# Kernel optimization log

Measured on AMD Instinct MI355X. Metric: run time of the kernel, lower is better.

## Reference

```python
import jax, jax.numpy as jnp
import numpy as np

B, C, IMG, PS, S, D, H, HD, L, OUT = 512, 3, 36, 6, 36, 768, 12, 64, 4, 256

def _pos_embedding(seq_len, dim):
    # NOTE: cos at even indices, sin at odd (as in the torch source)
    position = np.arange(seq_len, dtype=np.float32)[:, None]
    div = np.exp(np.arange(0, dim, 2, dtype=np.float32) * -(np.log(10000.0) / dim))
    emb = np.zeros((seq_len, dim), dtype=np.float32)
    emb[:, 0::2] = np.cos(position * div)
    emb[:, 1::2] = np.sin(position * div)
    return jnp.asarray(emb)

def setup_inputs():
    ks = jax.random.split(jax.random.key(0), 10)
    sc = lambda f: 1.0 / np.sqrt(f)
    return {
        'batch': jax.random.normal(ks[0], (B, C, IMG, IMG), jnp.float32),
        'W_patch': jax.random.normal(ks[1], (D, PS * PS), jnp.float32) * sc(PS * PS),
        'b_patch': jnp.zeros((D,), jnp.float32),
        'pos': _pos_embedding(S, D),
        'ln1_g': jnp.ones((L, D), jnp.float32),
        'ln1_b': jnp.zeros((L, D), jnp.float32),
        'Wq': jax.random.normal(ks[2], (L, H, HD, HD), jnp.float32) * sc(HD),
        'bq': jnp.zeros((L, H, HD), jnp.float32),
        'Wk': jax.random.normal(ks[3], (L, H, HD, HD), jnp.float32) * sc(HD),
        'bk': jnp.zeros((L, H, HD), jnp.float32),
        'Wv': jax.random.normal(ks[4], (L, H, HD, HD), jnp.float32) * sc(HD),
        'bv': jnp.zeros((L, H, HD), jnp.float32),
        'ln2_g': jnp.ones((L, D), jnp.float32),
        'ln2_b': jnp.zeros((L, D), jnp.float32),
        'W1': jax.random.normal(ks[5], (L, 2 * D, D), jnp.float32) * sc(D),
        'b1': jnp.zeros((L, 2 * D), jnp.float32),
        'W2': jax.random.normal(ks[6], (L, D, 2 * D), jnp.float32) * sc(2 * D),
        'b2': jnp.zeros((L, D), jnp.float32),
        'W_out': jax.random.normal(ks[7], (OUT, D), jnp.float32) * sc(D),
        'b_out': jnp.zeros((OUT,), jnp.float32),
    }

def _layernorm(x, g, b):
    m = jnp.mean(x, axis=-1, keepdims=True)
    v = jnp.mean((x - m) ** 2, axis=-1, keepdims=True)
    return (x - m) / jnp.sqrt(v + 1e-5) * g + b

def _forward(batch, W_patch, b_patch, pos, ln1_g, ln1_b, Wq, bq, Wk, bk, Wv, bv,
             ln2_g, ln2_b, W1, b1, W2, b2, W_out, b_out):
    b_, c_ = batch.shape[0], batch.shape[1]
    # patchify: (B,C,36,36) -> (B,C,36 patches,36 pixels), matching torch unfold+reshape
    p = batch.reshape(b_, c_, IMG // PS, PS, IMG // PS, PS)
    p = p.transpose(0, 1, 2, 4, 3, 5).reshape(b_, c_, S, PS * PS)
    z = p @ W_patch.T + b_patch + pos  # pos broadcasts over (B,C)
    scale = 1.0 / np.sqrt(HD)
    for l in range(L):
        # pre-LN then batched per-head attention (collapses the python loops)
        h = _layernorm(z, ln1_g[l], ln1_b[l]).reshape(b_, c_, S, H, HD)
        q = jnp.einsum('bcshd,hed->bcshe', h, Wq[l]) + bq[l]
        k = jnp.einsum('bcshd,hed->bcshe', h, Wk[l]) + bk[l]
        v = jnp.einsum('bcshd,hed->bcshe', h, Wv[l]) + bv[l]
        attn = jax.nn.softmax(jnp.einsum('bcshe,bcthe->bchst', q, k) * scale, axis=-1)
        o = jnp.einsum('bchst,bcthe->bcshe', attn, v).reshape(b_, c_, S, D)
        z = z + o
        z = _layernorm(z, ln2_g[l], ln2_b[l])
        z = z + (jax.nn.relu(z @ W1[l].T + b1[l]) @ W2[l].T + b2[l])
    return z @ W_out.T + b_out

def reference(batch, W_patch, b_patch, pos, ln1_g, ln1_b, Wq, bq, Wk, bk, Wv, bv,
              ln2_g, ln2_b, W1, b1, W2, b2, W_out, b_out):
    return _forward(batch, W_patch, b_patch, pos, ln1_g, ln1_b, Wq, bq, Wk, bk, Wv, bv,
                    ln2_g, ln2_b, W1, b1, W2, b2, W_out, b_out)
```

## Files before the change

### kernel.cpp

```cpp
#include <hip/hip_runtime.h>
#include <hip/hip_bf16.h>
#include <cstdint>
#include <cstddef>

typedef __bf16 bf16;
typedef bf16 bf16x8 __attribute__((ext_vector_type(8)));
typedef bf16 bf16x4 __attribute__((ext_vector_type(4)));
typedef float f32x4 __attribute__((ext_vector_type(4)));
typedef unsigned int u32;

#define GLD_LDS16(gptr, lptr)                                                        \
  __builtin_amdgcn_global_load_lds((const __attribute__((address_space(1))) u32*)(gptr), \
                                   (__attribute__((address_space(3))) u32*)(lptr), 16, 0, 0)

static constexpr int S = 36, D = 768, H = 12, HD = 64, DFF = 1536;
static constexpr int BC = 1536;
static constexpr int M = BC * S;
static constexpr int OUTD = 256;

__global__ __launch_bounds__(256) void f2b_kernel(const float* __restrict__ in,
                                                  bf16* __restrict__ out, int n4) {
  int i = blockIdx.x * 256 + threadIdx.x;
  if (i < n4) {
    float4 f = ((const float4*)in)[i];
    bf16x4 o = {(bf16)f.x, (bf16)f.y, (bf16)f.z, (bf16)f.w};
    ((bf16x4*)out)[i] = o;
  }
}

__global__ __launch_bounds__(64) void qk_prep(const float* __restrict__ Wq,
                                              const float* __restrict__ Wk,
                                              const float* __restrict__ bq,
                                              bf16* __restrict__ wb,
                                              float* __restrict__ vkout) {
  int lh = blockIdx.x;
  int e = threadIdx.x;
  __shared__ float Wqs[64][64];
  __shared__ float Wks[64][64];
  const float* wqp = Wq + (size_t)lh * 4096;
  const float* wkp = Wk + (size_t)lh * 4096;
  for (int i = e; i < 4096; i += 64) {
    Wqs[i >> 6][i & 63] = wqp[i];
    Wks[i >> 6][i & 63] = wkp[i];
  }
  __syncthreads();
  float ks[64];
#pragma unroll
  for (int f = 0; f < 64; ++f) ks[f] = Wks[f][e];
  for (int d0 = 0; d0 < 64; d0 += 4) {
    float a0 = 0.f, a1 = 0.f, a2 = 0.f, a3 = 0.f;
#pragma unroll
    for (int f = 0; f < 64; ++f) {
      float4 wq4 = *(const float4*)&Wqs[f][d0];
      a0 += wq4.x * ks[f]; a1 += wq4.y * ks[f];
      a2 += wq4.z * ks[f]; a3 += wq4.w * ks[f];
    }
    bf16x4 o = {(bf16)a0, (bf16)a1, (bf16)a2, (bf16)a3};
    *(bf16x4*)&wb[(size_t)lh * 4096 + e * 64 + d0] = o;
  }
  const float* bqp = bq + lh * 64;
  float acc = 0.f;
#pragma unroll
  for (int f = 0; f < 64; ++f) acc += ks[f] * bqp[f];
  vkout[lh * 64 + e] = acc;
}

__global__ __launch_bounds__(256) void patch_embed(const float* __restrict__ batch,
                                                   const float* __restrict__ Wp,
                                                   const float* __restrict__ bp,
                                                   const float* __restrict__ pos,
                                                   float* __restrict__ z) {
  int bc = blockIdx.x, tid = threadIdx.x;
  __shared__ float p[36][40];
  for (int i = tid; i < 1296; i += 256) {
    float f = batch[(size_t)bc * 1296 + i];
    int row = i / 36, col = i - row * 36;
    p[(row / 6) * 6 + col / 6][(row % 6) * 6 + (col % 6)] = f;
  }
  __syncthreads();
  for (int c0 = 0; c0 < 768; c0 += 256) {
    int d = c0 + tid;
    float wr[36];
    const float4* wp4 = (const float4*)(Wp + (size_t)d * 36);
#pragma unroll
    for (int q = 0; q < 9; ++q) {
      float4 f = wp4[q];
      wr[q * 4] = f.x; wr[q * 4 + 1] = f.y; wr[q * 4 + 2] = f.z; wr[q * 4 + 3] = f.w;
    }
    float gb = bp[d];
    for (int s = 0; s < 36; ++s) {
      float acc = 0.f;
#pragma unroll
      for (int k = 0; k < 36; ++k) acc += p[s][k] * wr[k];
      z[((size_t)bc * 36 + s) * 768 + d] = acc + gb + pos[s * 768 + d];
    }
  }
}

__global__ __launch_bounds__(256) void ln_stats(const float* __restrict__ zin,
                                                float* __restrict__ stats) {
  int row = blockIdx.x * 4 + (threadIdx.x >> 6);
  int lane = threadIdx.x & 63;
  const float* zr = zin + (size_t)row * D;
  float x[12];
#pragma unroll
  for (int i = 0; i < 12; ++i) x[i] = zr[i * 64 + lane];
  float s = 0.f;
#pragma unroll
  for (int i = 0; i < 12; ++i) s += x[i];
#pragma unroll
  for (int off = 32; off >= 1; off >>= 1) s += __shfl_xor(s, off, 64);
  float m = s * (1.f / 768.f);
  float v = 0.f;
#pragma unroll
  for (int i = 0; i < 12; ++i) { float dd = x[i] - m; v += dd * dd; }
#pragma unroll
  for (int off = 32; off >= 1; off >>= 1) v += __shfl_xor(v, off, 64);
  v *= (1.f / 768.f);
  if (lane == 0) {
    stats[(size_t)row * 2] = m;
    stats[(size_t)row * 2 + 1] = rsqrtf(v + 1e-5f);
  }
}

__global__ __launch_bounds__(256) void ln_inplace(float* __restrict__ z,
                                                  const float* __restrict__ g,
                                                  const float* __restrict__ bt,
                                                  bf16* __restrict__ zb) {
  int row = blockIdx.x * 4 + (threadIdx.x >> 6);
  int lane = threadIdx.x & 63;
  float* zr = z + (size_t)row * D;
  float x[12];
#pragma unroll
  for (int i = 0; i < 12; ++i) x[i] = zr[i * 64 + lane];
  float s = 0.f;
#pragma unroll
  for (int i = 0; i < 12; ++i) s += x[i];
#pragma unroll
  for (int off = 32; off >= 1; off >>= 1) s += __shfl_xor(s, off, 64);
  float m = s * (1.f / 768.f);
  float v = 0.f;
#pragma unroll
  for (int i = 0; i < 12; ++i) { float dd = x[i] - m; v += dd * dd; }
#pragma unroll
  for (int off = 32; off >= 1; off >>= 1) v += __shfl_xor(v, off, 64);
  v *= (1.f / 768.f);
  float rstd = rsqrtf(v + 1e-5f);
  bf16* zbr = zb ? zb + (size_t)row * D : nullptr;
#pragma unroll
  for (int i = 0; i < 12; ++i) {
    int d = i * 64 + lane;
    float o = (x[i] - m) * rstd * g[d] + bt[d];
    zr[d] = o;
    if (zbr) zbr[d] = (bf16)o;
  }
}

__global__ __launch_bounds__(64) void attn_kernel(const float* __restrict__ zg,
                                                  const float* __restrict__ stats,
                                                  const float* __restrict__ g1,
                                                  const float* __restrict__ b1_,
                                                  const bf16* __restrict__ Wqk,
                                                  const bf16* __restrict__ Wv,
                                                  const float* __restrict__ vk,
                                                  const float* __restrict__ bv,
                                                  float* __restrict__ z) {
  int head = blockIdx.x;
  int bc = blockIdx.y;
  __shared__ __align__(16) bf16 gb[48 * 72];
  __shared__ __align__(16) bf16 vt[64 * 72];
  int lane = threadIdx.x;
  int lr = lane & 15, quad = lane >> 4;

#pragma unroll
  for (int t0 = 0; t0 < 16; ++t0) vt[lane * 72 + 48 + t0] = (bf16)0.f;

  const float* zsrc = zg + ((size_t)bc * S) * D + head * HD;
  const float* st = stats + (size_t)bc * S * 2;

  float gv[2][8], bvv[2][8];
#pragma unroll
  for (int kt = 0; kt < 2; ++kt) {
    int c0 = head * HD + kt * 32 + quad * 8;
    float4 ga = *(const float4*)(g1 + c0);
    float4 gb2 = *(const float4*)(g1 + c0 + 4);
    float4 ba = *(const float4*)(b1_ + c0);
    float4 bb2 = *(const float4*)(b1_ + c0 + 4);
    gv[kt][0] = ga.x; gv[kt][1] = ga.y; gv[kt][2] = ga.z; gv[kt][3] = ga.w;
    gv[kt][4] = gb2.x; gv[kt][5] = gb2.y; gv[kt][6] = gb2.z; gv[kt][7] = gb2.w;
    bvv[kt][0] = ba.x; bvv[kt][1] = ba.y; bvv[kt][2] = ba.z; bvv[kt][3] = ba.w;
    bvv[kt][4] = bb2.x; bvv[kt][5] = bb2.y; bvv[kt][6] = bb2.z; bvv[kt][7] = bb2.w;
  }

  bf16x8 hfrag[3][2];
#pragma unroll
  for (int mt = 0; mt < 3; ++mt) {
    int srow = mt * 16 + lr;
    if (srow < 36) {
      float mm = st[srow * 2], rr = st[srow * 2 + 1];
#pragma unroll
      for (int kt = 0; kt < 2; ++kt) {
        int c0 = kt * 32 + quad * 8;
        float4 f0 = *(const float4*)(zsrc + (size_t)srow * D + c0);
        float4 f1 = *(const float4*)(zsrc + (size_t)srow * D + c0 + 4);
        float hv[8] = {f0.x, f0.y, f0.z, f0.w, f1.x, f1.y, f1.z, f1.w};
        bf16x8 o;
#pragma unroll
        for (int j = 0; j < 8; ++j) o[j] = (bf16)((hv[j] - mm) * rr * gv[kt][j] + bvv[kt][j]);
        hfrag[mt][kt] = o;
      }
    } else {
#pragma unroll
      for (int kt = 0; kt < 2; ++kt) {
        bf16x8 o;
#pragma unroll
        for (int j = 0; j < 8; ++j) o[j] = (bf16)0.f;
        hfrag[mt][kt] = o;
      }
    }
  }

  float vkv[2][8];
#pragma unroll
  for (int kt = 0; kt < 2; ++kt) {
    int c0 = head * 64 + kt * 32 + quad * 8;
    float4 va = *(const float4*)(vk + c0);
    float4 vb2 = *(const float4*)(vk + c0 + 4);
    vkv[kt][0] = va.x; vkv[kt][1] = va.y; vkv[kt][2] = va.z; vkv[kt][3] = va.w;
    vkv[kt][4] = vb2.x; vkv[kt][5] = vb2.y; vkv[kt][6] = vb2.z; vkv[kt][7] = vb2.w;
  }
  float tv[3];
#pragma unroll
  for (int mt = 0; mt < 3; ++mt) {
    float sp = 0.f;
#pragma unroll
    for (int kt = 0; kt < 2; ++kt)
#pragma unroll
      for (int j = 0; j < 8; ++j) sp += (float)hfrag[mt][kt][j] * vkv[kt][j];
    sp += __shfl_xor(sp, 16, 64);
    sp += __shfl_xor(sp, 32, 64);
    tv[mt] = sp;
  }

  const bf16* Wm[2] = {Wqk + (size_t)head * 4096, Wv + (size_t)head * 4096};
  const float* bvp = bv + head * 64;
  for (int p = 0; p < 2; ++p) {
    bf16x8 bfr[4][2];
#pragma unroll
    for (int nt = 0; nt < 4; ++nt)
#pragma unroll
      for (int kt = 0; kt < 2; ++kt)
        bfr[nt][kt] = *(const bf16x8*)(Wm[p] + (nt * 16 + lr) * 64 + kt * 32 + quad * 8);
#pragma unroll
    for (int mt = 0; mt < 3; ++mt) {
      f32x4 acc[4] = {};
#pragma unroll
      for (int kt = 0; kt < 2; ++kt)
#pragma unroll
        for (int nt = 0; nt < 4; ++nt)
          acc[nt] = __builtin_amdgcn_mfma_f32_16x16x32_bf16(hfrag[mt][kt], bfr[nt][kt], acc[nt], 0, 0, 0);
#pragma unroll
      for (int nt = 0; nt < 4; ++nt) {
        float bb = (p == 1) ? bvp[nt * 16 + lr] : 0.f;
#pragma unroll
        for (int r = 0; r < 4; ++r) {
          int s2 = mt * 16 + quad * 4 + r;
          int e = nt * 16 + lr;
          float val = acc[nt][r] + bb;
          if (p == 0) gb[s2 * 72 + e] = (bf16)val;
          else vt[e * 72 + s2] = (bf16)val;
        }
      }
    }
  }
  __syncthreads();

  f32x4 sc[3][3];
#pragma unroll
  for (int mt = 0; mt < 3; ++mt)
#pragma unroll
    for (int nt = 0; nt < 3; ++nt) {
      f32x4 a = {};
#pragma unroll
      for (int kt = 0; kt < 2; ++kt) {
        bf16x8 af = *(const bf16x8*)&gb[(mt * 16 + lr) * 72 + kt * 32 + quad * 8];
        a = __builtin_amdgcn_mfma_f32_16x16x32_bf16(af, hfrag[nt][kt], a, 0, 0, 0);
      }
      int t = nt * 16 + lr;
#pragma unroll
      for (int r = 0; r < 4; ++r) {
        float v = (a[r] + tv[nt]) * 0.125f;
        if (t >= 36) v = -1e30f;
        sc[mt][nt][r] = v;
      }
    }
  __syncthreads();

#pragma unroll
  for (int mt = 0; mt < 3; ++mt) {
    float mx[4], sum[4];
#pragma unroll
    for (int r = 0; r < 4; ++r)
      mx[r] = fmaxf(fmaxf(sc[mt][0][r], sc[mt][1][r]), sc[mt][2][r]);
#pragma unroll
    for (int r = 0; r < 4; ++r)
#pragma unroll
      for (int off = 8; off >= 1; off >>= 1) mx[r] = fmaxf(mx[r], __shfl_xor(mx[r], off, 64));
#pragma unroll
    for (int r = 0; r < 4; ++r) sum[r] = 0.f;
#pragma unroll
    for (int nt = 0; nt < 3; ++nt)
#pragma unroll
      for (int r = 0; r < 4; ++r) {
        float e = __expf(sc[mt][nt][r] - mx[r]);
        sc[mt][nt][r] = e;
        sum[r] += e;
      }
#pragma unroll
    for (int r = 0; r < 4; ++r)
#pragma unroll
      for (int off = 8; off >= 1; off >>= 1) sum[r] += __shfl_xor(sum[r], off, 64);
#pragma unroll
    for (int nt = 0; nt < 4; ++nt)
#pragma unroll
      for (int r = 0; r < 4; ++r) {
        int s2 = mt * 16 + quad * 4 + r;
        int t = nt * 16 + lr;
        float pv = (nt < 3) ? sc[mt][nt][r] / sum[r] : 0.f;
        gb[s2 * 72 + t] = (bf16)pv;
      }
  }
  __syncthreads();

#pragma unroll
  for (int mt = 0; mt < 3; ++mt) {
    f32x4 o[4] = {};
#pragma unroll
    for (int kt = 0; kt < 2; ++kt) {
      bf16x8 a = *(const bf16x8*)&gb[(mt * 16 + lr) * 72 + kt * 32 + quad * 8];
#pragma unroll
      for (int nt = 0; nt < 4; ++nt) {
        bf16x8 b = *(const bf16x8*)&vt[(nt * 16 + lr) * 72 + kt * 32 + quad * 8];
        o[nt] = __builtin_amdgcn_mfma_f32_16x16x32_bf16(a, b, o[nt], 0, 0, 0);
      }
    }
#pragma unroll
    for (int nt = 0; nt < 4; ++nt)
#pragma unroll
      for (int r = 0; r < 4; ++r) {
        int s2 = mt * 16 + quad * 4 + r;
        if (s2 < 36) {
          int e = nt * 16 + lr;
          size_t idx = ((size_t)bc * S + s2) * D + head * HD + e;
          z[idx] += o[nt][r];
        }
      }
  }
}

template <int N, int K, int MODE, int AF32>
__global__ __launch_bounds__(256) void gemm_bt(const void* __restrict__ A,
                                               const bf16* __restrict__ Bw,
                                               const float* __restrict__ bias,
                                               const float* __restrict__ res,
                                               void* __restrict__ outp) {
  constexpr int BK = 64;
  __shared__ __align__(16) bf16 As[128 * BK];
  __shared__ __align__(16) bf16 Bs[128 * BK];
  int tid = threadIdx.x;
  int bn = blockIdx.x, bm = blockIdx.y;
  const bf16* Abf = (const bf16*)A + (size_t)bm * 128 * K;
  const float* Af = (const float*)A + (size_t)bm * 128 * K;
  const bf16* Bb = Bw + (size_t)bn * 128 * K;
  int lane = tid & 63, wave = tid >> 6;
  int wm = (wave >> 1) * 64, wn = (wave & 1) * 64;
  int lr = lane & 15, quad = lane >> 4;
  f32x4 acc[4][4] = {};
  for (int k0 = 0; k0 < K; k0 += BK) {
    if (AF32) {
#pragma unroll
      for (int r = 0; r < 8; ++r) {
        int c = r * 256 + tid;
        int row = c >> 4, col4 = (c & 15) * 4;
        float4 f = *(const float4*)(Af + (size_t)row * K + k0 + col4);
        bf16x4 o = {(bf16)f.x, (bf16)f.y, (bf16)f.z, (bf16)f.w};
        *(bf16x4*)&As[row * BK + col4] = o;
      }
    } else {
#pragma unroll
      for (int r = 0; r < 4; ++r) {
        int c = r * 256 + tid;
        int row = c >> 3, col = (c & 7) * 8;
        GLD_LDS16(Abf + (size_t)row * K + k0 + col, &As[c * 8]);
      }
    }
#pragma unroll
    for (int r = 0; r < 4; ++r) {
      int c = r * 256 + tid;
      int row = c >> 3, col = (c & 7) * 8;
      GLD_LDS16(Bb + (size_t)row * K + k0 + col, &Bs[c * 8]);
    }
    __syncthreads();
#pragma unroll
    for (int kt = 0; kt < 2; ++kt) {
      bf16x8 af[4], bfr[4];
#pragma unroll
      for (int mt = 0; mt < 4; ++mt) af[mt] = *(const bf16x8*)&As[(wm + mt * 16 + lr) * BK + kt * 32 + quad * 8];
#pragma unroll
      for (int nt = 0; nt < 4; ++nt) bfr[nt] = *(const bf16x8*)&Bs[(wn + nt * 16 + lr) * BK + kt * 32 + quad * 8];
#pragma unroll
      for (int mt = 0; mt < 4; ++mt)
#pragma unroll
        for (int nt = 0; nt < 4; ++nt)
          acc[mt][nt] = __builtin_amdgcn_mfma_f32_16x16x32_bf16(af[mt], bfr[nt], acc[mt][nt], 0, 0, 0);
    }
    __syncthreads();
  }
  int row0 = bm * 128 + wm + quad * 4;
  int col0 = bn * 128 + wn + lr;
#pragma unroll
  for (int mt = 0; mt < 4; ++mt)
#pragma unroll
    for (int nt = 0; nt < 4; ++nt) {
      int col = col0 + nt * 16;
      float bv = bias[col];
#pragma unroll
      for (int r = 0; r < 4; ++r) {
        size_t idx = (size_t)(row0 + mt * 16 + r) * N + col;
        float v = acc[mt][nt][r] + bv;
        if (MODE == 0) ((bf16*)outp)[idx] = (bf16)fmaxf(v, 0.f);
        else if (MODE == 1) ((float*)outp)[idx] = v + res[idx];
        else ((float*)outp)[idx] = v;
      }
    }
}

extern "C" void kernel_launch(void* const* d_in, const int* in_sizes, int n_in,
                              void* d_out, int out_size, void* d_ws, size_t ws_size,
                              hipStream_t stream) {
  const float* batch   = (const float*)d_in[0];
  const float* W_patch = (const float*)d_in[1];
  const float* b_patch = (const float*)d_in[2];
  const float* pos     = (const float*)d_in[3];
  const float* ln1_g   = (const float*)d_in[4];
  const float* ln1_b   = (const float*)d_in[5];
  const float* Wq      = (const float*)d_in[6];
  const float* bq      = (const float*)d_in[7];
  const float* Wk      = (const float*)d_in[8];
  const float* bk      = (const float*)d_in[9];
  const float* Wv      = (const float*)d_in[10];
  const float* bv      = (const float*)d_in[11];
  const float* ln2_g   = (const float*)d_in[12];
  const float* ln2_b   = (const float*)d_in[13];
  const float* W1      = (const float*)d_in[14];
  const float* b1      = (const float*)d_in[15];
  const float* W2      = (const float*)d_in[16];
  const float* b2      = (const float*)d_in[17];
  const float* W_out   = (const float*)d_in[18];
  const float* b_out   = (const float*)d_in[19];
  float* out = (float*)d_out;
  (void)bk;

  char* ws = (char*)d_ws;
  size_t off = 0;
  float* z     = (float*)(ws + off); off += (size_t)M * D * 4;
  float* stats = (float*)(ws + off); off += (size_t)M * 2 * 4;
  bf16* wqk_b = (bf16*)(ws + off);   off += (size_t)4 * H * 4096 * 2;
  bf16* wv_b = (bf16*)(ws + off);    off += (size_t)4 * H * 4096 * 2;
  float* vk_f = (float*)(ws + off);  off += (size_t)4 * H * 64 * 4;
  bf16* w1_b = (bf16*)(ws + off);    off += (size_t)4 * DFF * D * 2;
  bf16* w2_b = (bf16*)(ws + off);    off += (size_t)4 * D * DFF * 2;
  bf16* wo_b = (bf16*)(ws + off);    off += (size_t)OUTD * D * 2;

  size_t avail = ws_size > off ? ws_size - off : (size_t)0;
  long long rcl = (long long)(avail / ((size_t)(DFF + D) * 2));
  int rc = (rcl > (long long)M) ? M : (int)rcl;
  rc = (rc / 128) * 128;
  if (rc <= 0) rc = 128;
  bf16* act = (bf16*)(ws + off);  off += (size_t)rc * DFF * 2;
  bf16* zbc = (bf16*)(ws + off);

  qk_prep<<<48, 64, 0, stream>>>(Wq, Wk, bq, wqk_b, vk_f);
  f2b_kernel<<<192, 256, 0, stream>>>(Wv, wv_b, 49152);
  f2b_kernel<<<4608, 256, 0, stream>>>(W1, w1_b, 1179648);
  f2b_kernel<<<4608, 256, 0, stream>>>(W2, w2_b, 1179648);
  f2b_kernel<<<192, 256, 0, stream>>>(W_out, wo_b, 49152);

  patch_embed<<<BC, 256, 0, stream>>>(batch, W_patch, b_patch, pos, z);

  for (int l = 0; l < 4; ++l) {
    ln_stats<<<M / 4, 256, 0, stream>>>(z, stats);
    attn_kernel<<<dim3(H, BC), 64, 0, stream>>>(z, stats, ln1_g + l * D, ln1_b + l * D,
        wqk_b + (size_t)l * H * 4096, wv_b + (size_t)l * H * 4096,
        vk_f + (size_t)l * H * 64, bv + (size_t)l * H * 64, z);
    for (int m0 = 0; m0 < M; m0 += rc) {
      int mr = (M - m0 < rc) ? (M - m0) : rc;
      ln_inplace<<<mr / 4, 256, 0, stream>>>(z + (size_t)m0 * D, ln2_g + l * D,
                                             ln2_b + l * D, zbc);
      gemm_bt<DFF, D, 0, 0><<<dim3(DFF / 128, mr / 128), 256, 0, stream>>>(
          zbc, w1_b + (size_t)l * DFF * D, b1 + l * DFF, nullptr, act);
      gemm_bt<D, DFF, 1, 0><<<dim3(D / 128, mr / 128), 256, 0, stream>>>(
          act, w2_b + (size_t)l * D * DFF, b2 + l * D, z + (size_t)m0 * D,
          z + (size_t)m0 * D);
    }
  }

  gemm_bt<OUTD, D, 2, 1><<<dim3(OUTD / 128, M / 128), 256, 0, stream>>>(
      z, wo_b, b_out, nullptr, out);
}
```

Before: 3.470 ms.

## Double-buffer A tile in LDS and load B fragments directly from global

The GEMM kernel now double-buffers the A tile in shared memory, prefetching the next K-step while the current one is computed, so one barrier per step is dropped. The B (weight) tile is no longer staged in LDS; each wave reads its B fragments straight from global memory into registers. This aims to overlap A loads with MFMA work and halve LDS traffic. The cost is that B is read redundantly by the two wave rows, with uncoalesced strided 16-byte global loads that depend on cache hits, and register pressure goes up.

```diff
diff --git a/kernel.cpp b/kernel.cpp
--- a/kernel.cpp
+++ b/kernel.cpp
@@ -365,8 +365,8 @@
                                                const float* __restrict__ res,
                                                void* __restrict__ outp) {
   constexpr int BK = 64;
-  __shared__ __align__(16) bf16 As[128 * BK];
-  __shared__ __align__(16) bf16 Bs[128 * BK];
+  constexpr int NSTEP = K / BK;
+  __shared__ __align__(16) bf16 As[2][128 * BK];
   int tid = threadIdx.x;
   int bn = blockIdx.x, bm = blockIdx.y;
   const bf16* Abf = (const bf16*)A + (size_t)bm * 128 * K;
@@ -375,8 +375,8 @@
   int lane = tid & 63, wave = tid >> 6;
   int wm = (wave >> 1) * 64, wn = (wave & 1) * 64;
   int lr = lane & 15, quad = lane >> 4;
-  f32x4 acc[4][4] = {};
-  for (int k0 = 0; k0 < K; k0 += BK) {
+
+  auto stageA = [&](int buf, int k0) {
     if (AF32) {
 #pragma unroll
       for (int r = 0; r < 8; ++r) {
@@ -384,35 +384,42 @@
         int row = c >> 4, col4 = (c & 15) * 4;
         float4 f = *(const float4*)(Af + (size_t)row * K + k0 + col4);
         bf16x4 o = {(bf16)f.x, (bf16)f.y, (bf16)f.z, (bf16)f.w};
-        *(bf16x4*)&As[row * BK + col4] = o;
+        *(bf16x4*)&As[buf][row * BK + col4] = o;
       }
     } else {
 #pragma unroll
       for (int r = 0; r < 4; ++r) {
         int c = r * 256 + tid;
         int row = c >> 3, col = (c & 7) * 8;
-        GLD_LDS16(Abf + (size_t)row * K + k0 + col, &As[c * 8]);
-      }
-    }
-#pragma unroll
-    for (int r = 0; r < 4; ++r) {
-      int c = r * 256 + tid;
-      int row = c >> 3, col = (c & 7) * 8;
-      GLD_LDS16(Bb + (size_t)row * K + k0 + col, &Bs[c * 8]);
-    }
-    __syncthreads();
+        GLD_LDS16(Abf + (size_t)row * K + k0 + col, &As[buf][c * 8]);
+      }
+    }
+  };
+
+  f32x4 acc[4][4] = {};
+  stageA(0, 0);
+  __syncthreads();
+  for (int s = 0; s < NSTEP; ++s) {
+    int cur = s & 1;
+    if (s + 1 < NSTEP) stageA(cur ^ 1, (s + 1) * BK);
+    int k0 = s * BK;
+    bf16x8 bfr[4][2];
+#pragma unroll
+    for (int nt = 0; nt < 4; ++nt)
+#pragma unroll
+      for (int kt = 0; kt < 2; ++kt)
+        bfr[nt][kt] = *(const bf16x8*)(Bb + (size_t)(wn + nt * 16 + lr) * K + k0 + kt * 32 + quad * 8);
 #pragma unroll
     for (int kt = 0; kt < 2; ++kt) {
-      bf16x8 af[4], bfr[4];
-#pragma unroll
-      for (int mt = 0; mt < 4; ++mt) af[mt] = *(const bf16x8*)&As[(wm + mt * 16 + lr) * BK + kt * 32 + quad * 8];
-#pragma unroll
-      for (int nt = 0; nt < 4; ++nt) bfr[nt] = *(const bf16x8*)&Bs[(wn + nt * 16 + lr) * BK + kt * 32 + quad * 8];
+      bf16x8 af[4];
 #pragma unroll
       for (int mt = 0; mt < 4; ++mt)
+        af[mt] = *(const bf16x8*)&As[cur][(wm + mt * 16 + lr) * BK + kt * 32 + quad * 8];
+#pragma unroll
+      for (int mt = 0; mt < 4; ++mt)
 #pragma unroll
         for (int nt = 0; nt < 4; ++nt)
-          acc[mt][nt] = __builtin_amdgcn_mfma_f32_16x16x32_bf16(af[mt], bfr[nt], acc[mt][nt], 0, 0, 0);
+          acc[mt][nt] = __builtin_amdgcn_mfma_f32_16x16x32_bf16(af[mt], bfr[nt][kt], acc[mt][nt], 0, 0, 0);
     }
     __syncthreads();
   }
```

Result: slower. 4.497 ms (+29.6%).
